# Performance work log

Hardware: AMD Instinct MI355X
Metric: run time of the kernel (lower is better)

Reference implementation:

```python
import jax, jax.numpy as jnp
import numpy as np

FT = 0.2  # clip floor (init arg ft)

def _norm_mat(m):
    # matrix / (count of nonzeros along last dim + 1e-30)
    deg = jnp.sum(m != 0, axis=-1, keepdims=True).astype(m.dtype)
    return m / (deg + 1e-30)

def _l2n(x):
    return x / (jnp.linalg.norm(x, axis=-1, keepdims=True) + 1e-30)

def setup_inputs():
    B, L, D, H, O = 2, 2048, 64, 64, 128
    N = 2 * L
    ks = jax.random.split(jax.random.key(0), 30)
    u = lambda i, s: jax.random.uniform(ks[i], s, jnp.float32)
    g = lambda i, s: jax.random.normal(ks[i], s, jnp.float32) * 0.05
    inp = {}
    inp['word_outputs_0'] = g(0, (B, L, D))
    inp['word_outputs_1'] = g(1, (B, L, D))
    inp['node_hidden'] = g(2, (B, D))
    inp['op_embedding'] = g(3, (B, O, D))
    inp['word_exist_sequence'] = (u(4, (B, N)) < 0.8).astype(jnp.float32)
    inp['word_exist_matrix'] = (u(5, (B, N, N)) < 0.8).astype(jnp.float32)
    inp['word_operator'] = (u(6, (B, N, O)) < 0.02).astype(jnp.float32)
    inp['word_word'] = (u(7, (B, N, N)) < 0.01).astype(jnp.float32)
    inp['depend_0'] = (u(8, (B, L, L)) < 0.05).astype(jnp.float32)
    inp['depend_1'] = (u(9, (B, L, L)) < 0.05).astype(jnp.float32)
    inp['goal_word'] = u(10, (B, N))
    names = [('Wg', (D, H)), ('bg', (H,)), ('Wwk', (D, H)), ('bwk', (H,)),
             ('Wws', (D, H)), ('bws', (H,)), ('Wo', (D, D)), ('bo', (D,)),
             ('Wupd', (3 * H, D)), ('bupd', (D,)), ('Wf', (3 * H + D, D)), ('bf', (D,)),
             ('Wf2', (2 * D, D)), ('bf2', (D,)), ('Wout', (D, D)), ('bout', (D,))]
    for i, (nm, s) in enumerate(names):
        inp[nm] = g(11 + i, s)
    return inp

def _forward(w0, w1, nh, opE, wes, wem, wop, ww, d0, d1, gw,
             Wg, bg, Wwk, bwk, Wws, bws, Wo, bo, Wupd, bupd, Wf, bf, Wf2, bf2, Wout, bout):
    all_w = jnp.concatenate([w0, w1], axis=1)                      # [B,N,D]
    goal_trans = (nh @ Wg + bg)[:, None, :]                        # [B,1,H] (broadcast = expand)
    word_g = _l2n(goal_trans * gw[..., None])                      # [B,N,H]
    word_w_k = _l2n(jnp.matmul(_norm_mat(ww * wem), all_w @ Wwk + bwk))
    ws0 = jnp.matmul(_norm_mat(d0), w0 @ Wws + bws)
    ws1 = jnp.matmul(_norm_mat(d1), w1 @ Wws + bws)
    word_w_s = _l2n(jnp.concatenate([ws0, ws1], axis=1))           # [B,N,H]
    neigh = jnp.concatenate([word_g, word_w_k, word_w_s], axis=-1)  # [B,N,3H]
    forget = jax.nn.sigmoid(jnp.concatenate([all_w, word_g, word_w_k, word_w_s], axis=-1) @ Wf + bf)
    word_updated = jnp.maximum(forget, FT) * all_w + (1.0 - forget) * jax.nn.relu(neigh @ Wupd + bupd)
    adj_op = _norm_mat(jnp.swapaxes(wes[..., None] * wop, 1, 2))   # [B,O,N]
    word_op = jnp.matmul(adj_op, word_updated @ Wo + bo)           # [B,O,D]
    forget2 = jax.nn.sigmoid(jnp.concatenate([opE, word_op], axis=-1) @ Wf2 + bf2)
    op_out = jnp.maximum(forget2, FT) * opE + (1.0 - forget2) * jax.nn.relu(word_op @ Wout + bout)
    # original returns (split(word_updated), op_embedding); concat along node axis here
    return jnp.concatenate([word_updated, op_out], axis=1)         # [B,N+O,D]

def reference(word_outputs_0, word_outputs_1, node_hidden, op_embedding,
              word_exist_sequence, word_exist_matrix, word_operator, word_word,
              depend_0, depend_1, goal_word,
              Wg, bg, Wwk, bwk, Wws, bws, Wo, bo, Wupd, bupd, Wf, bf, Wf2, bf2, Wout, bout):
    return _forward(word_outputs_0, word_outputs_1, node_hidden, op_embedding,
                    word_exist_sequence, word_exist_matrix, word_operator, word_word,
                    depend_0, depend_1, goal_word,
                    Wg, bg, Wwk, bwk, Wws, bws, Wo, bo, Wupd, bupd, Wf, bf, Wf2, bf2, Wout, bout)
```

## Files before the change

### kernel.cpp

```cpp
#include <hip/hip_runtime.h>
#include <cstdint>

typedef unsigned short u16;
typedef unsigned long long u64;
typedef __attribute__((ext_vector_type(8))) short bf16x8;
typedef __attribute__((ext_vector_type(4))) float f32x4;

__device__ __forceinline__ u16 f2b(float f){
  union { float f; uint32_t i; } v; v.f = f;
  uint32_t r = v.i + 0x7FFFu + ((v.i >> 16) & 1u);
  return (u16)(r >> 16);
}
__device__ __forceinline__ float b2f(u16 u){
  union { uint32_t i; float f; } v; v.i = ((uint32_t)u) << 16; return v.f;
}
__device__ __forceinline__ float sigmoidf(float x){ return 1.0f / (1.0f + __expf(-x)); }

#define MFMA16(a,b,c) __builtin_amdgcn_mfma_f32_16x16x32_bf16(a,b,c,0,0,0)

__global__ __launch_bounds__(256) void k_prep(
    const float* __restrict__ w0, const float* __restrict__ w1,
    u16* __restrict__ wThi, u16* __restrict__ wTlo){
  __shared__ float tile[64][65];
  int tid = threadIdx.x;
  int t = blockIdx.x;
  int b = t >> 6, kt = t & 63;
  int k0 = kt * 64;
  const float* src = (k0 < 2048) ? (w0 + ((size_t)b*2048 + k0)*64)
                                 : (w1 + ((size_t)b*2048 + (k0 - 2048))*64);
  int r0 = tid >> 6, c = tid & 63;
  #pragma unroll
  for (int it = 0; it < 16; ++it){
    int n = it*4 + r0;
    tile[n][c] = src[(size_t)n*64 + c];
  }
  __syncthreads();
  #pragma unroll
  for (int it = 0; it < 16; ++it){
    int d = it*4 + r0;
    float v = tile[c][d];
    u16 h = f2b(v);
    float lo = v - b2f(h);
    size_t o = ((size_t)b*64 + d)*4096 + k0 + c;
    wThi[o] = h;
    wTlo[o] = f2b(lo);
  }
}

__global__ __launch_bounds__(256) void k_mask(
    const float* __restrict__ ww, const float* __restrict__ wem,
    const float* __restrict__ d0, const float* __restrict__ d1,
    const float* __restrict__ wes, const float* __restrict__ wop,
    const u16* __restrict__ wThi, const u16* __restrict__ wTlo,
    const float* __restrict__ nh, const float* __restrict__ Wg, const float* __restrict__ bg,
    const float* __restrict__ Wf, const float* __restrict__ Wupd, const float* __restrict__ Wo,
    u16* __restrict__ psumB, int* __restrict__ pcntB,
    u16* __restrict__ psumD, int* __restrict__ pcntD,
    u64* __restrict__ bitOp, float* __restrict__ ghat,
    uint32_t* __restrict__ pkWf, uint32_t* __restrict__ pkWu, uint32_t* __restrict__ pkWo){
  int tid = threadIdx.x, wave = tid >> 6, lane = tid & 63;
  int bid = blockIdx.x;
  if (bid >= 768){
    if (bid >= 1024){
      int aux = bid - 1024;
      if (aux == 16){
        if (tid < 128){
          int b = tid >> 6, h = tid & 63;
          float g = bg[h];
          for (int d = 0; d < 64; ++d) g += nh[b*64 + d] * Wg[d*64 + h];
          float ss = g * g;
          #pragma unroll
          for (int o = 32; o > 0; o >>= 1) ss += __shfl_xor(ss, o, 64);
          ghat[b*64 + h] = g / (sqrtf(ss) + 1e-30f);
        }
        return;
      }
      for (int k = tid; k < 1024; k += 256){
        int i = aux*1024 + k;
        const float* src; uint32_t* dst; int li;
        if (i < 8192){ src = Wf; dst = pkWf; li = i; }
        else if (i < 14336){ src = Wupd; dst = pkWu; li = i - 8192; }
        else { src = Wo; dst = pkWo; li = i - 14336; }
        int k2 = li >> 6, ln = li & 63;
        dst[li] = (uint32_t)f2b(src[(2*k2)*64 + ln]) | ((uint32_t)f2b(src[(2*k2+1)*64 + ln]) << 16);
      }
      return;
    }
    int w = (bid - 768)*4 + wave;
    int ng0 = w * 8;
    #pragma unroll
    for (int i = 0; i < 8; ++i){
      int n = ng0 + i;
      float vx = wop[(size_t)n*128 + lane];
      float vy = wop[(size_t)n*128 + 64 + lane];
      float e  = wes[n];
      u64 m0 = __ballot((e != 0.f) && (vx != 0.f));
      u64 m1 = __ballot((e != 0.f) && (vy != 0.f));
      if (lane == 0) bitOp[(size_t)n*2]     = m0;
      if (lane == 1) bitOp[(size_t)n*2 + 1] = m1;
    }
    return;
  }
  bool big; int wb, kOffW, tBase, tStride;
  const float *mArow, *mBrow; size_t ldm;
  u16* psArr; int* pcArr;
  if (bid < 512){
    int rowblk = bid >> 2, kq = bid & 3;
    int bb = rowblk >> 6;
    int grow = bb*4096 + (rowblk & 63)*64 + wave*16;
    mArow = ww  + (size_t)grow*4096 + kq*1024;
    mBrow = wem + (size_t)grow*4096 + kq*1024;
    ldm = 4096; big = true;
    wb = bb; kOffW = kq*1024;
    tBase = grow*4 + kq; tStride = 4;
    psArr = psumB; pcArr = pcntB;
  } else {
    int i = bid - 512;
    int inst = i >> 6, r6 = i & 63;
    int rowblkL = r6 >> 1, kh = r6 & 1;
    int prow = inst*2048 + rowblkL*64 + wave*16;
    const float* marr = (inst < 2) ? d0 : d1;
    int mrow = (inst < 2) ? prow : (prow - 4096);
    mArow = marr + (size_t)mrow*2048 + kh*1024;
    mBrow = mArow; ldm = 2048; big = false;
    wb = inst & 1; kOffW = ((inst >= 2) ? 2048 : 0) + kh*1024;
    tBase = prow*2 + kh; tStride = 2;
    psArr = psumD; pcArr = pcntD;
  }
  int col = lane & 15, oct = lane >> 4;
  const float* pa = mArow + (size_t)col*ldm + oct*8;
  const float* pc = mBrow + (size_t)col*ldm + oct*8;
  const u16* ph = wThi + ((size_t)wb*64 + col)*4096 + kOffW + oct*8;
  const u16* pl = wTlo + ((size_t)wb*64 + col)*4096 + kOffW + oct*8;

  f32x4 acc0 = {0.f,0.f,0.f,0.f}, acc1 = acc0, acc2 = acc0, acc3 = acc0, accD = acc0;
  union { uint32_t w[4]; bf16x8 v; } onesU;
  onesU.w[0] = onesU.w[1] = onesU.w[2] = onesU.w[3] = 0x3F803F80u;
  bf16x8 ones = onesU.v;

  float4 a0 = *(const float4*)pa;
  float4 a1 = *(const float4*)(pa + 4);
  float4 c0v = {0,0,0,0}, c1v = {0,0,0,0};
  if (big){ c0v = *(const float4*)pc; c1v = *(const float4*)(pc + 4); }
  bf16x8 h0 = *(const bf16x8*)ph;
  bf16x8 h1 = *(const bf16x8*)(ph + 65536);
  bf16x8 h2 = *(const bf16x8*)(ph + 131072);
  bf16x8 h3 = *(const bf16x8*)(ph + 196608);
  bf16x8 l0 = *(const bf16x8*)pl;
  bf16x8 l1 = *(const bf16x8*)(pl + 65536);
  bf16x8 l2 = *(const bf16x8*)(pl + 131072);
  bf16x8 l3 = *(const bf16x8*)(pl + 196608);

  #pragma unroll 1
  for (int s = 0; s < 32; ++s){
    float4 wa0 = a0, wa1 = a1, wc0 = c0v, wc1 = c1v;
    bf16x8 bh0 = h0, bh1 = h1, bh2 = h2, bh3 = h3;
    bf16x8 bl0 = l0, bl1 = l1, bl2 = l2, bl3 = l3;
    if (s < 31){
      const float* qa = pa + (size_t)(s+1)*32;
      a0 = *(const float4*)qa; a1 = *(const float4*)(qa + 4);
      if (big){
        const float* qc = pc + (size_t)(s+1)*32;
        c0v = *(const float4*)qc; c1v = *(const float4*)(qc + 4);
      }
      const u16* qh = ph + (size_t)(s+1)*32;
      h0 = *(const bf16x8*)qh;
      h1 = *(const bf16x8*)(qh + 65536);
      h2 = *(const bf16x8*)(qh + 131072);
      h3 = *(const bf16x8*)(qh + 196608);
      const u16* ql = pl + (size_t)(s+1)*32;
      l0 = *(const bf16x8*)ql;
      l1 = *(const bf16x8*)(ql + 65536);
      l2 = *(const bf16x8*)(ql + 131072);
      l3 = *(const bf16x8*)(ql + 196608);
    }
#define SEL(x,y) ((x != 0.f) && (!big || (y != 0.f)))
    union { uint32_t w[4]; bf16x8 v; } af;
    af.w[0] = (SEL(wa0.x,wc0.x)?0x3F80u:0u) | (SEL(wa0.y,wc0.y)?0x3F800000u:0u);
    af.w[1] = (SEL(wa0.z,wc0.z)?0x3F80u:0u) | (SEL(wa0.w,wc0.w)?0x3F800000u:0u);
    af.w[2] = (SEL(wa1.x,wc1.x)?0x3F80u:0u) | (SEL(wa1.y,wc1.y)?0x3F800000u:0u);
    af.w[3] = (SEL(wa1.z,wc1.z)?0x3F80u:0u) | (SEL(wa1.w,wc1.w)?0x3F800000u:0u);
#undef SEL
    bf16x8 a = af.v;
    acc0 = MFMA16(a, bh0, acc0);
    acc0 = MFMA16(a, bl0, acc0);
    acc1 = MFMA16(a, bh1, acc1);
    acc1 = MFMA16(a, bl1, acc1);
    acc2 = MFMA16(a, bh2, acc2);
    acc2 = MFMA16(a, bl2, acc2);
    acc3 = MFMA16(a, bh3, acc3);
    acc3 = MFMA16(a, bl3, acc3);
    accD = MFMA16(a, ones, accD);
  }
  #pragma unroll
  for (int r = 0; r < 4; ++r){
    size_t t = (size_t)tBase + (size_t)(oct*4 + r) * tStride;
    u16* prow = psArr + t*64;
    prow[ 0 + col] = f2b(acc0[r]);
    prow[16 + col] = f2b(acc1[r]);
    prow[32 + col] = f2b(acc2[r]);
    prow[48 + col] = f2b(acc3[r]);
    if (col == 0) pcArr[t] = (int)(accD[r] + 0.5f);
  }
}

__global__ __launch_bounds__(256) void k_fin(
    const u16* __restrict__ psumB, const int* __restrict__ pcntB,
    const u16* __restrict__ psumD, const int* __restrict__ pcntD,
    const float* __restrict__ Wwk, const float* __restrict__ bwk,
    const float* __restrict__ Wws, const float* __restrict__ bws,
    u16* __restrict__ wwkn, u16* __restrict__ wwsn){
  __shared__ float sWk[4096], sWs[4096];
  int tid = threadIdx.x, lane = tid & 63, wave = tid >> 6;
  for (int i = tid; i < 1024; i += 256){
    ((float4*)sWk)[i] = ((const float4*)Wwk)[i];
    ((float4*)sWs)[i] = ((const float4*)Wws)[i];
  }
  __syncthreads();
  for (int r = 0; r < 4; ++r){
    int wid = blockIdx.x*4 + wave + r*4096;
    float S; float y; const float* sW; u16* outp; size_t oidx;
    if (wid < 8192){
      S = b2f(psumB[((size_t)wid*4 + 0)*64 + lane]) + b2f(psumB[((size_t)wid*4 + 1)*64 + lane])
        + b2f(psumB[((size_t)wid*4 + 2)*64 + lane]) + b2f(psumB[((size_t)wid*4 + 3)*64 + lane]);
      int T = pcntB[wid*4] + pcntB[wid*4 + 1] + pcntB[wid*4 + 2] + pcntB[wid*4 + 3];
      y = (float)T * bwk[lane]; sW = sWk; outp = wwkn; oidx = wid;
    } else {
      int rp = wid - 8192;
      S = b2f(psumD[((size_t)rp*2 + 0)*64 + lane]) + b2f(psumD[((size_t)rp*2 + 1)*64 + lane]);
      int T = pcntD[rp*2] + pcntD[rp*2 + 1];
      y = (float)T * bws[lane]; sW = sWs; outp = wwsn;
      int b, n;
      if (rp < 4096){ b = rp >> 11; n = rp & 2047; }
      else { int rr = rp - 4096; b = rr >> 11; n = 2048 + (rr & 2047); }
      oidx = (size_t)b*4096 + n;
    }
    #pragma unroll 8
    for (int d = 0; d < 64; ++d) y += __shfl(S, d, 64) * sW[d*64 + lane];
    float ss = y * y;
    #pragma unroll
    for (int o = 32; o > 0; o >>= 1) ss += __shfl_xor(ss, o, 64);
    outp[oidx*64 + lane] = f2b(y / (sqrtf(ss) + 1e-30f));
  }
}

__global__ __launch_bounds__(256, 2) void k_update(
    const float* __restrict__ w0, const float* __restrict__ w1,
    const float* __restrict__ gw, const float* __restrict__ ghat,
    const u16* __restrict__ wwkn, const u16* __restrict__ wwsn,
    const uint32_t* __restrict__ pkWf, const uint32_t* __restrict__ pkWu,
    const uint32_t* __restrict__ pkWo,
    const float* __restrict__ bf, const float* __restrict__ bupd, const float* __restrict__ bo,
    float* __restrict__ out, float* __restrict__ WUo){
  __shared__ uint32_t pWf[8192];
  __shared__ uint32_t pWu[6144];
  __shared__ uint32_t pWo[2048];
  __shared__ float xsh[4][256];
  int tid = threadIdx.x;
  for (int i = tid; i < 2048; i += 256) ((uint4*)pWf)[i] = ((const uint4*)pkWf)[i];
  for (int i = tid; i < 1536; i += 256) ((uint4*)pWu)[i] = ((const uint4*)pkWu)[i];
  for (int i = tid; i < 512;  i += 256) ((uint4*)pWo)[i] = ((const uint4*)pkWo)[i];
  __syncthreads();
  int lane = tid & 63, wave = tid >> 6;
  float bff = bf[lane], bup = bupd[lane], boo = bo[lane];
  float aw[4], wgv[4], wk[4], wsv[4];
  #pragma unroll
  for (int t = 0; t < 4; ++t){
    int row = blockIdx.x*4 + wave + t*2048;
    int b = row >> 12, n = row & 4095;
    aw[t] = (n < 2048) ? w0[((size_t)(b*2048 + n))*64 + lane]
                       : w1[((size_t)(b*2048 + n - 2048))*64 + lane];
    float gvv = gw[b*4096 + n];
    wgv[t] = (gvv != 0.f) ? ghat[b*64 + lane] : 0.f;
    wk[t]  = b2f(wwkn[(size_t)row*64 + lane]);
    wsv[t] = b2f(wwsn[(size_t)row*64 + lane]);
  }
  #pragma unroll
  for (int t = 0; t < 4; ++t){
    int row = blockIdx.x*4 + wave + t*2048;
    int b = row >> 12, n = row & 4095;
    xsh[wave][lane] = aw[t]; xsh[wave][64 + lane] = wgv[t];
    xsh[wave][128 + lane] = wk[t]; xsh[wave][192 + lane] = wsv[t];
    float f = bff, u = bup;
    #pragma unroll 8
    for (int k2 = 0; k2 < 32; ++k2){
      float2 xv = *(const float2*)&xsh[wave][2*k2];
      uint32_t wf = pWf[k2*64 + lane];
      f += xv.x * b2f((u16)wf) + xv.y * b2f((u16)(wf >> 16));
    }
    #pragma unroll 8
    for (int k2 = 32; k2 < 128; ++k2){
      float2 xv = *(const float2*)&xsh[wave][2*k2];
      uint32_t wf = pWf[k2*64 + lane];
      uint32_t wu = pWu[(k2 - 32)*64 + lane];
      f += xv.x * b2f((u16)wf) + xv.y * b2f((u16)(wf >> 16));
      u += xv.x * b2f((u16)wu) + xv.y * b2f((u16)(wu >> 16));
    }
    f = sigmoidf(f);
    u = fmaxf(u, 0.f);
    float wu = fmaxf(f, 0.2f) * aw[t] + (1.f - f) * u;
    out[((size_t)b*4224 + n)*64 + lane] = wu;
    float o = boo;
    #pragma unroll 8
    for (int k2 = 0; k2 < 32; ++k2){
      uint32_t wo2 = pWo[k2*64 + lane];
      o += __shfl(wu, 2*k2, 64) * b2f((u16)wo2) + __shfl(wu, 2*k2 + 1, 64) * b2f((u16)(wo2 >> 16));
    }
    WUo[(size_t)row*64 + lane] = o;
  }
}

__global__ __launch_bounds__(256) void k_opfin(
    const u64* __restrict__ bitOp, const float* __restrict__ WUo,
    const float* __restrict__ opE,
    const float* __restrict__ Wf2, const float* __restrict__ bf2,
    const float* __restrict__ Wout, const float* __restrict__ bout,
    float* __restrict__ out){
  __shared__ float sW2[8192];
  __shared__ float sWo[4096];
  __shared__ int q[4][96];
  __shared__ float sacc[4][64];
  __shared__ int scnt[4];
  __shared__ float xsh[128];
  int tid = threadIdx.x, lane = tid & 63, wave = tid >> 6;
  for (int i = tid; i < 2048; i += 256) ((float4*)sW2)[i] = ((const float4*)Wf2)[i];
  for (int i = tid; i < 1024; i += 256) ((float4*)sWo)[i] = ((const float4*)Wout)[i];
  int rowIdx = blockIdx.x;
  int b = rowIdx >> 7, o = rowIdx & 127;
  int wrd = o >> 6, bit = o & 63;
  const u64* bp = bitOp + (size_t)b*8192 + (size_t)wave*2048 + wrd;
  u64 lt = (1ULL << lane) - 1ULL;
  u64 vv[16];
  #pragma unroll
  for (int it = 0; it < 16; ++it) vv[it] = bp[(size_t)(it*64 + lane)*2];
  int cnt = 0;
  #pragma unroll
  for (int it = 0; it < 16; ++it){
    bool nz = (vv[it] >> bit) & 1ULL;
    u64 m = __ballot(nz);
    if (nz) q[wave][cnt + (int)__popcll(m & lt)] = wave*1024 + it*64 + lane;
    cnt += (int)__popcll(m);
  }
  const float* Xb = WUo + (size_t)b*4096*64 + lane;
  float acc = 0.f;
  int i = 0;
  for (; i + 8 <= cnt; i += 8){
    int4 c0 = *(const int4*)&q[wave][i];
    int4 c1 = *(const int4*)&q[wave][i + 4];
    float v0 = Xb[(size_t)c0.x*64], v1 = Xb[(size_t)c0.y*64];
    float v2 = Xb[(size_t)c0.z*64], v3 = Xb[(size_t)c0.w*64];
    float v4 = Xb[(size_t)c1.x*64], v5 = Xb[(size_t)c1.y*64];
    float v6 = Xb[(size_t)c1.z*64], v7 = Xb[(size_t)c1.w*64];
    acc += ((v0 + v1) + (v2 + v3)) + ((v4 + v5) + (v6 + v7));
  }
  for (; i < cnt; ++i) acc += Xb[(size_t)q[wave][i]*64];
  sacc[wave][lane] = acc;
  if (lane == 0) scnt[wave] = cnt;
  __syncthreads();
  if (wave == 0){
    float t = sacc[0][lane] + sacc[1][lane] + sacc[2][lane] + sacc[3][lane];
    float deg = (float)(scnt[0] + scnt[1] + scnt[2] + scnt[3]);
    float wo = t / (deg + 1e-30f);
    float e  = opE[(size_t)rowIdx*64 + lane];
    xsh[lane] = e; xsh[64 + lane] = wo;
    float f = bf2[lane], u = bout[lane];
    #pragma unroll 8
    for (int k = 0; k < 128; ++k) f += xsh[k] * sW2[k*64 + lane];
    #pragma unroll 8
    for (int d = 0; d < 64; ++d)  u += xsh[64 + d] * sWo[d*64 + lane];
    f = sigmoidf(f);
    u = fmaxf(u, 0.f);
    float res = fmaxf(f, 0.2f) * e + (1.f - f) * u;
    out[((size_t)b*4224 + 4096 + o)*64 + lane] = res;
  }
}

extern "C" void kernel_launch(void* const* d_in, const int* in_sizes, int n_in,
                              void* d_out, int out_size, void* d_ws, size_t ws_size,
                              hipStream_t stream){
  const float* w0   = (const float*)d_in[0];
  const float* w1   = (const float*)d_in[1];
  const float* nh   = (const float*)d_in[2];
  const float* opE  = (const float*)d_in[3];
  const float* wes  = (const float*)d_in[4];
  const float* wem  = (const float*)d_in[5];
  const float* wop  = (const float*)d_in[6];
  const float* ww   = (const float*)d_in[7];
  const float* d0   = (const float*)d_in[8];
  const float* d1   = (const float*)d_in[9];
  const float* gw   = (const float*)d_in[10];
  const float* Wg   = (const float*)d_in[11];
  const float* bg   = (const float*)d_in[12];
  const float* Wwk  = (const float*)d_in[13];
  const float* bwk  = (const float*)d_in[14];
  const float* Wws  = (const float*)d_in[15];
  const float* bws  = (const float*)d_in[16];
  const float* Wo   = (const float*)d_in[17];
  const float* bo   = (const float*)d_in[18];
  const float* Wupd = (const float*)d_in[19];
  const float* bupd = (const float*)d_in[20];
  const float* Wf   = (const float*)d_in[21];
  const float* bf   = (const float*)d_in[22];
  const float* Wf2  = (const float*)d_in[23];
  const float* bf2  = (const float*)d_in[24];
  const float* Wout = (const float*)d_in[25];
  const float* bout = (const float*)d_in[26];

  float* ws    = (float*)d_ws;
  float* ghat  = ws;
  uint32_t* pkWf = (uint32_t*)(ws + 128);
  uint32_t* pkWu = (uint32_t*)(ws + 8320);
  uint32_t* pkWo = (uint32_t*)(ws + 14464);
  u64*  bitOp  = (u64*)(ws + 16512);
  u16*  psumB  = (u16*)(ws + 49280);
  int*  pcntB  = (int*)(ws + 1097856);
  u16*  psumD  = (u16*)(ws + 1130624);
  int*  pcntD  = (int*)(ws + 1654912);
  u16*  wwkn   = (u16*)(ws + 1671296);
  u16*  wwsn   = (u16*)(ws + 1933440);
  float* WUo   = ws + 2195584;
  u16*  wThi   = (u16*)(ws + 2719872);
  u16*  wTlo   = (u16*)(ws + 2982016);
  float* out   = (float*)d_out;

  k_prep<<<128, 256, 0, stream>>>(w0, w1, wThi, wTlo);
  k_mask<<<1041, 256, 0, stream>>>(ww, wem, d0, d1, wes, wop, wThi, wTlo,
                                   nh, Wg, bg, Wf, Wupd, Wo,
                                   psumB, pcntB, psumD, pcntD,
                                   bitOp, ghat, pkWf, pkWu, pkWo);
  k_fin<<<1024, 256, 0, stream>>>(psumB, pcntB, psumD, pcntD,
                                  Wwk, bwk, Wws, bws, wwkn, wwsn);
  k_update<<<512, 256, 0, stream>>>(w0, w1, gw, ghat, wwkn, wwsn,
                                    pkWf, pkWu, pkWo, bf, bupd, bo, out, WUo);
  k_opfin<<<256, 256, 0, stream>>>(bitOp, WUo, opE, Wf2, bf2, Wout, bout, out);
}
```

Measured before the change: 492.2 us.

## Load mask rows coalesced, ballot into LDS bitmasks, permute k-order of transposed words

The masked-adjacency matmul kernel used to read mask rows with strided per-lane float4 loads (16 rows, 8 floats per lane). It now has each wave read whole rows with coalesced float4 loads and compress them into 64-bit ballot bitmasks stored in LDS. The MFMA loop then reads one byte per step to build the 0/1 bf16 A fragment. To keep the bit order consistent, the prep kernel writes the transposed word hi/lo arrays in a permuted k-order that matches the ballot layout. This targets the cost of uncoalesced global reads of the large dense masks, and adds a preload phase and LDS use per block.

```diff
diff --git a/kernel.cpp b/kernel.cpp
--- a/kernel.cpp
+++ b/kernel.cpp
@@ -2,6 +2,7 @@
 #include <cstdint>
 
 typedef unsigned short u16;
+typedef unsigned char u8;
 typedef unsigned long long u64;
 typedef __attribute__((ext_vector_type(8))) short bf16x8;
 typedef __attribute__((ext_vector_type(4))) float f32x4;
@@ -35,13 +36,16 @@
     tile[n][c] = src[(size_t)n*64 + c];
   }
   __syncthreads();
+  int j  = k0 + c;
+  int jl = j & 1023;
+  int kap = (j & ~1023) + ((jl >> 8) << 8) + ((jl & 3) << 6) + ((jl >> 2) & 63);
   #pragma unroll
   for (int it = 0; it < 16; ++it){
     int d = it*4 + r0;
     float v = tile[c][d];
     u16 h = f2b(v);
     float lo = v - b2f(h);
-    size_t o = ((size_t)b*64 + d)*4096 + k0 + c;
+    size_t o = ((size_t)b*64 + d)*4096 + kap;
     wThi[o] = h;
     wTlo[o] = f2b(lo);
   }
@@ -58,6 +62,7 @@
     u16* __restrict__ psumD, int* __restrict__ pcntD,
     u64* __restrict__ bitOp, float* __restrict__ ghat,
     uint32_t* __restrict__ pkWf, uint32_t* __restrict__ pkWu, uint32_t* __restrict__ pkWo){
+  __shared__ u64 sb[4][272];
   int tid = threadIdx.x, wave = tid >> 6, lane = tid & 63;
   int bid = blockIdx.x;
   if (bid >= 768){
@@ -128,20 +133,50 @@
     psArr = psumD; pcArr = pcntD;
   }
   int col = lane & 15, oct = lane >> 4;
-  const float* pa = mArow + (size_t)col*ldm + oct*8;
-  const float* pc = mBrow + (size_t)col*ldm + oct*8;
+  u64* sbw = &sb[wave][0];
+  float4 a0, a1, a2, a3;
+  float4 b0v = {0,0,0,0}, b1v = {0,0,0,0}, b2v = {0,0,0,0}, b3v = {0,0,0,0};
+  {
+    const float4* ra = (const float4*)mArow + lane;
+    a0 = ra[0]; a1 = ra[64]; a2 = ra[128]; a3 = ra[192];
+    if (big){
+      const float4* rb = (const float4*)mBrow + lane;
+      b0v = rb[0]; b1v = rb[64]; b2v = rb[128]; b3v = rb[192];
+    }
+  }
+#define B4(i, va, vb) { \
+  u64 m0 = __ballot((va.x != 0.f) && (!big || (vb.x != 0.f))); \
+  u64 m1 = __ballot((va.y != 0.f) && (!big || (vb.y != 0.f))); \
+  u64 m2 = __ballot((va.z != 0.f) && (!big || (vb.z != 0.f))); \
+  u64 m3 = __ballot((va.w != 0.f) && (!big || (vb.w != 0.f))); \
+  if (lane == (i)*4 + 0) myw = m0; \
+  if (lane == (i)*4 + 1) myw = m1; \
+  if (lane == (i)*4 + 2) myw = m2; \
+  if (lane == (i)*4 + 3) myw = m3; }
+  #pragma unroll 1
+  for (int r = 0; r < 16; ++r){
+    float4 ca0 = a0, ca1 = a1, ca2 = a2, ca3 = a3;
+    float4 cb0 = b0v, cb1 = b1v, cb2 = b2v, cb3 = b3v;
+    if (r < 15){
+      const float4* ra = (const float4*)(mArow + (size_t)(r+1)*ldm) + lane;
+      a0 = ra[0]; a1 = ra[64]; a2 = ra[128]; a3 = ra[192];
+      if (big){
+        const float4* rb = (const float4*)(mBrow + (size_t)(r+1)*ldm) + lane;
+        b0v = rb[0]; b1v = rb[64]; b2v = rb[128]; b3v = rb[192];
+      }
+    }
+    u64 myw = 0;
+    B4(0, ca0, cb0) B4(1, ca1, cb1) B4(2, ca2, cb2) B4(3, ca3, cb3)
+    if (lane < 16) sbw[r*17 + lane] = myw;
+  }
+#undef B4
+  const u8* sbb = (const u8*)sbw;
   const u16* ph = wThi + ((size_t)wb*64 + col)*4096 + kOffW + oct*8;
   const u16* pl = wTlo + ((size_t)wb*64 + col)*4096 + kOffW + oct*8;
-
   f32x4 acc0 = {0.f,0.f,0.f,0.f}, acc1 = acc0, acc2 = acc0, acc3 = acc0, accD = acc0;
   union { uint32_t w[4]; bf16x8 v; } onesU;
   onesU.w[0] = onesU.w[1] = onesU.w[2] = onesU.w[3] = 0x3F803F80u;
   bf16x8 ones = onesU.v;
-
-  float4 a0 = *(const float4*)pa;
-  float4 a1 = *(const float4*)(pa + 4);
-  float4 c0v = {0,0,0,0}, c1v = {0,0,0,0};
-  if (big){ c0v = *(const float4*)pc; c1v = *(const float4*)(pc + 4); }
   bf16x8 h0 = *(const bf16x8*)ph;
   bf16x8 h1 = *(const bf16x8*)(ph + 65536);
   bf16x8 h2 = *(const bf16x8*)(ph + 131072);
@@ -150,37 +185,32 @@
   bf16x8 l1 = *(const bf16x8*)(pl + 65536);
   bf16x8 l2 = *(const bf16x8*)(pl + 131072);
   bf16x8 l3 = *(const bf16x8*)(pl + 196608);
-
+  uint32_t byn = sbb[col*136 + oct];
   #pragma unroll 1
   for (int s = 0; s < 32; ++s){
-    float4 wa0 = a0, wa1 = a1, wc0 = c0v, wc1 = c1v;
+    uint32_t by = byn;
     bf16x8 bh0 = h0, bh1 = h1, bh2 = h2, bh3 = h3;
     bf16x8 bl0 = l0, bl1 = l1, bl2 = l2, bl3 = l3;
     if (s < 31){
-      const float* qa = pa + (size_t)(s+1)*32;
-      a0 = *(const float4*)qa; a1 = *(const float4*)(qa + 4);
-      if (big){
-        const float* qc = pc + (size_t)(s+1)*32;
-        c0v = *(const float4*)qc; c1v = *(const float4*)(qc + 4);
-      }
-      const u16* qh = ph + (size_t)(s+1)*32;
+      int sn = s + 1;
+      int t4 = ((sn & 7) << 2) + oct;
+      byn = sbb[col*136 + (((sn >> 3) << 2) + (t4 >> 3))*8 + (t4 & 7)];
+      const u16* qh = ph + (size_t)sn*32;
       h0 = *(const bf16x8*)qh;
       h1 = *(const bf16x8*)(qh + 65536);
       h2 = *(const bf16x8*)(qh + 131072);
       h3 = *(const bf16x8*)(qh + 196608);
-      const u16* ql = pl + (size_t)(s+1)*32;
+      const u16* ql = pl + (size_t)sn*32;
       l0 = *(const bf16x8*)ql;
       l1 = *(const bf16x8*)(ql + 65536);
       l2 = *(const bf16x8*)(ql + 131072);
       l3 = *(const bf16x8*)(ql + 196608);
     }
-#define SEL(x,y) ((x != 0.f) && (!big || (y != 0.f)))
     union { uint32_t w[4]; bf16x8 v; } af;
-    af.w[0] = (SEL(wa0.x,wc0.x)?0x3F80u:0u) | (SEL(wa0.y,wc0.y)?0x3F800000u:0u);
-    af.w[1] = (SEL(wa0.z,wc0.z)?0x3F80u:0u) | (SEL(wa0.w,wc0.w)?0x3F800000u:0u);
-    af.w[2] = (SEL(wa1.x,wc1.x)?0x3F80u:0u) | (SEL(wa1.y,wc1.y)?0x3F800000u:0u);
-    af.w[3] = (SEL(wa1.z,wc1.z)?0x3F80u:0u) | (SEL(wa1.w,wc1.w)?0x3F800000u:0u);
-#undef SEL
+    af.w[0] = ((by &   1u) ? 0x3F80u : 0u) | ((by &   2u) ? 0x3F800000u : 0u);
+    af.w[1] = ((by &   4u) ? 0x3F80u : 0u) | ((by &   8u) ? 0x3F800000u : 0u);
+    af.w[2] = ((by &  16u) ? 0x3F80u : 0u) | ((by &  32u) ? 0x3F800000u : 0u);
+    af.w[3] = ((by &  64u) ? 0x3F80u : 0u) | ((by & 128u) ? 0x3F800000u : 0u);
     bf16x8 a = af.v;
     acc0 = MFMA16(a, bh0, acc0);
     acc0 = MFMA16(a, bl0, acc0);
```

After: 515.8 us. +4.8%, slower.
